# Kernel optimization log

Hardware: AMD Instinct MI355X
Metric: run time of the kernel (lower is better)

Reference implementation:

```python
import jax, jax.numpy as jnp
import numpy as np

EMB = 384
RANK = 8


def feature2token(f):
    # [B,C,H,W] -> [B,HW,C]
    B, C, H, W = f.shape
    return f.reshape(B, C, H * W).transpose(0, 2, 1)


def token2feature(t, H, W):
    # [B,N,C] -> [B,C,H,W]
    B, N, C = t.shape
    return t.transpose(0, 2, 1).reshape(B, C, H, W)


def linear(t, w, b):
    # torch Linear: y = t @ w.T + b ; w: [out,in]
    return jnp.einsum('bnc,oc->bno', t, w) + b


def hard_mask(y_soft, k):
    # straight-through one-hot mask of the top-k entries of y_soft, per row
    B, N = y_soft.shape
    idx = jax.lax.top_k(y_soft, k)[1]                      # [B,k]
    y_hard = jnp.zeros_like(y_soft).at[jnp.arange(B)[:, None], idx].set(1.0)
    return y_hard - jax.lax.stop_gradient(y_soft) + y_soft


def gumbel_masks(scores, k):
    # scores: [B,N] raw logits; module applies log_softmax then softmax
    y_soft = jax.nn.softmax(jax.nn.log_softmax(scores, axis=-1), axis=-1)
    token_mask = hard_mask(y_soft, k)        # top-k
    rej_mask = hard_mask(-y_soft, k) + 2.0 * jax.lax.stop_gradient(y_soft) - 2.0 * y_soft
    # note: rej uses topk of (-y_soft) for indices but straight-through around +y_soft,
    # so compute it directly for clarity:
    B, N = y_soft.shape
    idx_bot = jax.lax.top_k(-y_soft, k)[1]
    y_hard_bot = jnp.zeros_like(y_soft).at[jnp.arange(B)[:, None], idx_bot].set(1.0)
    rej_mask = y_hard_bot - jax.lax.stop_gradient(y_soft) + y_soft
    return token_mask, rej_mask


def setup_inputs() -> dict:
    key = jax.random.key(0)
    ks = jax.random.split(key, 20)
    B, C, H, W = 32, EMB, 32, 32
    s_emb = 1.0 / np.sqrt(EMB)
    s_2r = 1.0 / np.sqrt(2 * RANK)
    s_r = 1.0 / np.sqrt(RANK)
    inp = {
        'x': jax.random.normal(ks[0], (B, 2 * C, H, W), jnp.float32),
        'gx_w': jax.random.uniform(ks[1], (1, EMB), jnp.float32, -s_emb, s_emb),
        'gx_b': jax.random.uniform(ks[2], (1,), jnp.float32, -s_emb, s_emb),
        'gm_w': jax.random.uniform(ks[3], (1, EMB), jnp.float32, -s_emb, s_emb),
        'gm_b': jax.random.uniform(ks[4], (1,), jnp.float32, -s_emb, s_emb),
        'px_w': jax.random.uniform(ks[5], (RANK, EMB), jnp.float32, -s_emb, s_emb),
        'px_b': jax.random.uniform(ks[6], (RANK,), jnp.float32, -s_emb, s_emb),
        'pm_w': jax.random.uniform(ks[7], (RANK, EMB), jnp.float32, -s_emb, s_emb),
        'pm_b': jax.random.uniform(ks[8], (RANK,), jnp.float32, -s_emb, s_emb),
        'prx_w': jax.random.uniform(ks[9], (RANK, EMB), jnp.float32, -s_emb, s_emb),
        'prx_b': jax.random.uniform(ks[10], (RANK,), jnp.float32, -s_emb, s_emb),
        'prm_w': jax.random.uniform(ks[11], (RANK, EMB), jnp.float32, -s_emb, s_emb),
        'prm_b': jax.random.uniform(ks[12], (RANK,), jnp.float32, -s_emb, s_emb),
        'pfx_w': jax.random.uniform(ks[13], (RANK, 2 * RANK), jnp.float32, -s_2r, s_2r),
        'pfx_b': jax.random.uniform(ks[14], (RANK,), jnp.float32, -s_2r, s_2r),
        'pfm_w': jax.random.uniform(ks[15], (RANK, 2 * RANK), jnp.float32, -s_2r, s_2r),
        'pfm_b': jax.random.uniform(ks[16], (RANK,), jnp.float32, -s_2r, s_2r),
        'pb_w': jax.random.uniform(ks[17], (EMB, RANK), jnp.float32, -s_r, s_r),
        'pb_b': jax.random.uniform(ks[18], (EMB,), jnp.float32, -s_r, s_r),
    }
    return inp


def reference(x, gx_w, gx_b, gm_w, gm_b, px_w, px_b, pm_w, pm_b,
              prx_w, prx_b, prm_w, prm_b, pfx_w, pfx_b, pfm_w, pfm_b,
              pb_w, pb_b):
    xh, modh = jnp.split(x, 2, axis=1)           # each [B,C,H,W]
    H, W = xh.shape[2], xh.shape[3]
    xt = feature2token(xh)                        # [B,N,C]
    mt = feature2token(modh)
    B, N, _ = xt.shape
    k = N // 4

    # x-branch
    scores_x = linear(xt, gx_w, gx_b).reshape(B, N)
    tm_x, rm_x = gumbel_masks(scores_x, k)
    tm_x, rm_x = tm_x[..., None], rm_x[..., None]             # [B,N,1] broadcast over emb
    low_x = linear(xt * tm_x + mt * rm_x, px_w, px_b)
    low_res_x = linear((xt + mt) * (1.0 - rm_x - tm_x), prx_w, prx_b)
    fuse_x = linear(jnp.concatenate([low_x, low_res_x], axis=2), pfx_w, pfx_b)

    # mod-branch
    scores_m = linear(mt, gm_w, gm_b).reshape(B, N)
    tm_m, rm_m = gumbel_masks(scores_m, k)
    tm_m, rm_m = tm_m[..., None], rm_m[..., None]
    low_m = linear(mt * tm_m + xt * rm_m, pm_w, pm_b)
    low_res_m = linear((xt + mt) * (1.0 - rm_m - tm_m), prm_w, prm_b)
    fuse_m = linear(jnp.concatenate([low_m, low_res_m], axis=2), pfm_w, pfm_b)

    fuse = linear(fuse_x + fuse_m, pb_w, pb_b)   # [B,N,EMB]
    return token2feature(fuse, H, W)
```

## Files before the change

### kernel.cpp

```cpp
#include <hip/hip_runtime.h>

#define NTOK 1024
#define KSEL 256


template <int CS>
__global__ __launch_bounds__(128) void k1_proj(
    const float* __restrict__ x,
    const float* __restrict__ gx_w, const float* __restrict__ gm_w,
    const float* __restrict__ px_w, const float* __restrict__ pm_w,
    const float* __restrict__ prx_w, const float* __restrict__ prm_w,
    float* __restrict__ Pp)
{
  constexpr int NS = 384 / CS;
  constexpr int SB = (NS == 1) ? 0 : 2;
  constexpr int NCB = CS / 16;
  int blk = blockIdx.x;
  int part = blk & 1;
  int ntile = (blk >> 1) & 7;
  int s = (blk >> 4) & (NS - 1);
  int b = blk >> (4 + SB);
  int n = ntile * 128 + threadIdx.x;
  const float* gw = part ? gm_w : gx_w;
  int cw0 = s * CS;

  float acc[33];
  #pragma unroll
  for (int j = 0; j < 33; ++j) acc[j] = 0.f;

  const float* xp = x + ((size_t)b * 768 + part * 384 + cw0) * NTOK + n;

  float cur[16], nxt[16];
  #pragma unroll
  for (int i = 0; i < 16; ++i) cur[i] = xp[(size_t)i * NTOK];

  #pragma unroll
  for (int cb = 0; cb < NCB; ++cb) {
    #pragma unroll
    for (int i = 0; i < 16; ++i)
      nxt[i] = (cb + 1 < NCB) ? xp[(size_t)((cb + 1) * 16 + i) * NTOK] : 0.f;
    #pragma unroll
    for (int i = 0; i < 16; ++i) {
      int cw = cw0 + cb * 16 + i;
      float v = cur[i];
      acc[0] = fmaf(gw[cw], v, acc[0]);
      #pragma unroll
      for (int r = 0; r < 8; ++r) {
        acc[1 + r]  = fmaf(px_w[r * 384 + cw],  v, acc[1 + r]);
        acc[9 + r]  = fmaf(pm_w[r * 384 + cw],  v, acc[9 + r]);
        acc[17 + r] = fmaf(prx_w[r * 384 + cw], v, acc[17 + r]);
        acc[25 + r] = fmaf(prm_w[r * 384 + cw], v, acc[25 + r]);
      }
    }
    #pragma unroll
    for (int i = 0; i < 16; ++i) cur[i] = nxt[i];
  }
  float* op = Pp + ((((size_t)s * 32 + b) * 2 + part) * 33) * NTOK + n;
  #pragma unroll
  for (int j = 0; j < 33; ++j) op[(size_t)j * NTOK] = acc[j];
}

__global__ __launch_bounds__(64) void k2_masks(
    const float* __restrict__ Ppart, float* __restrict__ masks, int nsplit)
{
  int b = blockIdx.x >> 1;
  int branch = blockIdx.x & 1;
  int lane = threadIdx.x;
  unsigned long long lmask = (1ull << lane) - 1ull;

  float v[16];
  #pragma unroll
  for (int i = 0; i < 16; ++i) v[i] = 0.f;
  for (int s = 0; s < nsplit; ++s) {
    const float* sp = Ppart + (((size_t)s * 32 + b) * 2 + branch) * 33 * NTOK;
    #pragma unroll
    for (int i = 0; i < 16; ++i) v[i] += sp[i * 64 + lane];
  }
  unsigned key[16];
  #pragma unroll
  for (int i = 0; i < 16; ++i) {
    float f = v[i] + 0.0f;
    unsigned bits = __float_as_uint(f);
    key[i] = (bits & 0x80000000u) ? ~bits : (bits | 0x80000000u);
  }

  for (int which = 0; which < 2; ++which) {
    unsigned prefix = 0u;
    for (int bit = 31; bit >= 0; --bit) {
      unsigned cand = prefix | (1u << bit);
      int cnt = 0;
      #pragma unroll
      for (int i = 0; i < 16; ++i) {
        unsigned kk = which ? ~key[i] : key[i];
        cnt += __popcll(__ballot(kk >= cand));
      }
      if (cnt >= KSEL) prefix = cand;
    }
    int cgt = 0;
    #pragma unroll
    for (int i = 0; i < 16; ++i) {
      unsigned kk = which ? ~key[i] : key[i];
      cgt += __popcll(__ballot(kk > prefix));
    }
    int quota = KSEL - cgt;
    float* mp = masks + ((size_t)b * 4 + branch * 2 + which) * NTOK;
    int run = 0;
    #pragma unroll
    for (int i = 0; i < 16; ++i) {
      unsigned kk = which ? ~key[i] : key[i];
      bool eq = (kk == prefix);
      unsigned long long bal = __ballot(eq);
      int rank = run + __popcll(bal & lmask);
      bool sel = (kk > prefix) || (eq && rank < quota);
      mp[i * 64 + lane] = sel ? 1.0f : 0.0f;
      run += __popcll(bal);
    }
  }
}

template <int NS>
__global__ __launch_bounds__(1024) void k3a(
    const float* __restrict__ Ppart, const float* __restrict__ masks,
    const float* __restrict__ px_b, const float* __restrict__ pm_b,
    const float* __restrict__ prx_b, const float* __restrict__ prm_b,
    float* __restrict__ LOWS)
{
  int r = blockIdx.x & 7;
  int b = blockIdx.x >> 3;
  int n = threadIdx.x;

  float ax = 0.f, am = 0.f, bmv = 0.f, bxv = 0.f, cx = 0.f, cm = 0.f;
  #pragma unroll
  for (int s = 0; s < NS; ++s) {
    const float* P0 = Ppart + (((size_t)s * 32 + b) * 2 + 0) * 33 * NTOK + n;
    const float* P1 = Ppart + (((size_t)s * 32 + b) * 2 + 1) * 33 * NTOK + n;
    ax  += P0[(size_t)(1 + r) * NTOK];
    am  += P1[(size_t)(1 + r) * NTOK];
    bmv += P0[(size_t)(9 + r) * NTOK];
    bxv += P1[(size_t)(9 + r) * NTOK];
    cx  += P0[(size_t)(17 + r) * NTOK] + P1[(size_t)(17 + r) * NTOK];
    cm  += P0[(size_t)(25 + r) * NTOK] + P1[(size_t)(25 + r) * NTOK];
  }
  const float* mk = masks + (size_t)b * 4 * NTOK + n;
  float tmx = mk[0 * NTOK], rmx = mk[1 * NTOK];
  float tmm = mk[2 * NTOK], rmm = mk[3 * NTOK];
  float wx = 1.0f - tmx - rmx;
  float wm = 1.0f - tmm - rmm;

  float lowx = fmaf(tmx, ax, fmaf(rmx, am, px_b[r]));
  float lrx  = fmaf(wx, cx, prx_b[r]);
  float lowm = fmaf(tmm, bxv, fmaf(rmm, bmv, pm_b[r]));
  float lrm  = fmaf(wm, cm, prm_b[r]);

  float* L = LOWS + ((size_t)b * 32 + r) * NTOK + n;
  L[0 * 8 * NTOK] = lowx;
  L[1 * 8 * NTOK] = lrx;
  L[2 * 8 * NTOK] = lowm;
  L[3 * 8 * NTOK] = lrm;
}

__global__ __launch_bounds__(1024) void k3b(
    const float* __restrict__ LOWS,
    const float* __restrict__ pfx_w, const float* __restrict__ pfx_b,
    const float* __restrict__ pfm_w, const float* __restrict__ pfm_b,
    float* __restrict__ G)
{
  int b = blockIdx.x;
  int n = threadIdx.x;
  const float* L = LOWS + (size_t)b * 32 * NTOK + n;
  float lowx[8], lrx[8], lowm[8], lrm[8];
  #pragma unroll
  for (int r = 0; r < 8; ++r) {
    lowx[r] = L[(size_t)(0 * 8 + r) * NTOK];
    lrx[r]  = L[(size_t)(1 * 8 + r) * NTOK];
    lowm[r] = L[(size_t)(2 * 8 + r) * NTOK];
    lrm[r]  = L[(size_t)(3 * 8 + r) * NTOK];
  }
  float g[8];
  #pragma unroll
  for (int r = 0; r < 8; ++r) {
    float acc = pfx_b[r] + pfm_b[r];
    #pragma unroll
    for (int s2 = 0; s2 < 8; ++s2) {
      acc = fmaf(pfx_w[r * 16 + s2],     lowx[s2], acc);
      acc = fmaf(pfx_w[r * 16 + 8 + s2], lrx[s2],  acc);
      acc = fmaf(pfm_w[r * 16 + s2],     lowm[s2], acc);
      acc = fmaf(pfm_w[r * 16 + 8 + s2], lrm[s2],  acc);
    }
    g[r] = acc;
  }
  float4* Gp = reinterpret_cast<float4*>(G + ((size_t)b * NTOK + n) * 8);
  Gp[0] = make_float4(g[0], g[1], g[2], g[3]);
  Gp[1] = make_float4(g[4], g[5], g[6], g[7]);
}

__global__ __launch_bounds__(64) void k4_out(
    const float* __restrict__ G, const float* __restrict__ pb_w,
    const float* __restrict__ pb_b, float* __restrict__ out)
{
  int blk = blockIdx.x;
  int ttile = blk & 3;
  int cpart = (blk >> 2) & 3;
  int b = blk >> 4;
  int n0 = ttile * 256 + threadIdx.x * 4;

  const float4* Gp = reinterpret_cast<const float4*>(G + ((size_t)b * NTOK + n0) * 8);
  float4 ga0 = Gp[0], ga1 = Gp[1];
  float4 gb0 = Gp[2], gb1 = Gp[3];
  float4 gc0 = Gp[4], gc1 = Gp[5];
  float4 gd0 = Gp[6], gd1 = Gp[7];

  float* op = out + ((size_t)b * 384 + (size_t)cpart * 96) * NTOK + n0;
  const float* wp = pb_w + (size_t)cpart * 96 * 8;
  const float* bp = pb_b + (size_t)cpart * 96;
  #pragma unroll 4
  for (int c = 0; c < 96; ++c) {
    const float* w = wp + c * 8;
    float w0 = w[0], w1 = w[1], w2 = w[2], w3 = w[3];
    float w4 = w[4], w5 = w[5], w6 = w[6], w7 = w[7];
    float bb = bp[c];
    float4 o;
    o.x = bb; o.y = bb; o.z = bb; o.w = bb;
    o.x = fmaf(w0, ga0.x, o.x); o.x = fmaf(w1, ga0.y, o.x);
    o.x = fmaf(w2, ga0.z, o.x); o.x = fmaf(w3, ga0.w, o.x);
    o.x = fmaf(w4, ga1.x, o.x); o.x = fmaf(w5, ga1.y, o.x);
    o.x = fmaf(w6, ga1.z, o.x); o.x = fmaf(w7, ga1.w, o.x);
    o.y = fmaf(w0, gb0.x, o.y); o.y = fmaf(w1, gb0.y, o.y);
    o.y = fmaf(w2, gb0.z, o.y); o.y = fmaf(w3, gb0.w, o.y);
    o.y = fmaf(w4, gb1.x, o.y); o.y = fmaf(w5, gb1.y, o.y);
    o.y = fmaf(w6, gb1.z, o.y); o.y = fmaf(w7, gb1.w, o.y);
    o.z = fmaf(w0, gc0.x, o.z); o.z = fmaf(w1, gc0.y, o.z);
    o.z = fmaf(w2, gc0.z, o.z); o.z = fmaf(w3, gc0.w, o.z);
    o.z = fmaf(w4, gc1.x, o.z); o.z = fmaf(w5, gc1.y, o.z);
    o.z = fmaf(w6, gc1.z, o.z); o.z = fmaf(w7, gc1.w, o.z);
    o.w = fmaf(w0, gd0.x, o.w); o.w = fmaf(w1, gd0.y, o.w);
    o.w = fmaf(w2, gd0.z, o.w); o.w = fmaf(w3, gd0.w, o.w);
    o.w = fmaf(w4, gd1.x, o.w); o.w = fmaf(w5, gd1.y, o.w);
    o.w = fmaf(w6, gd1.z, o.w); o.w = fmaf(w7, gd1.w, o.w);
    *reinterpret_cast<float4*>(op + (size_t)c * NTOK) = o;
  }
}

extern "C" void kernel_launch(void* const* d_in, const int* in_sizes, int n_in,
                              void* d_out, int out_size, void* d_ws, size_t ws_size,
                              hipStream_t stream) {
  const float* x     = (const float*)d_in[0];
  const float* gx_w  = (const float*)d_in[1];
  const float* gm_w  = (const float*)d_in[3];
  const float* px_w  = (const float*)d_in[5];
  const float* px_b  = (const float*)d_in[6];
  const float* pm_w  = (const float*)d_in[7];
  const float* pm_b  = (const float*)d_in[8];
  const float* prx_w = (const float*)d_in[9];
  const float* prx_b = (const float*)d_in[10];
  const float* prm_w = (const float*)d_in[11];
  const float* prm_b = (const float*)d_in[12];
  const float* pfx_w = (const float*)d_in[13];
  const float* pfx_b = (const float*)d_in[14];
  const float* pfm_w = (const float*)d_in[15];
  const float* pfm_b = (const float*)d_in[16];
  const float* pb_w  = (const float*)d_in[17];
  const float* pb_b  = (const float*)d_in[18];
  float* out = (float*)d_out;

  const size_t P1_F   = 32ull * 2 * 33 * NTOK;
  const size_t MASK_F = 32ull * 4 * NTOK;
  const size_t G_F    = 32ull * NTOK * 8;
  const size_t LOWS_F = 32ull * 32 * NTOK;
  const size_t need4  = (4 * P1_F + MASK_F + G_F + LOWS_F) * 4;

  float* ws = (float*)d_ws;
  if (ws_size >= need4) {
    float* Ppart = ws;
    float* masks = ws + 4 * P1_F;
    float* G     = masks + MASK_F;
    float* LOWS  = G + G_F;
    k1_proj<96><<<2048, 128, 0, stream>>>(x, gx_w, gm_w, px_w, pm_w, prx_w, prm_w, Ppart);
    k2_masks<<<64, 64, 0, stream>>>(Ppart, masks, 4);
    k3a<4><<<256, 1024, 0, stream>>>(Ppart, masks, px_b, pm_b, prx_b, prm_b, LOWS);
    k3b<<<32, 1024, 0, stream>>>(LOWS, pfx_w, pfx_b, pfm_w, pfm_b, G);
    k4_out<<<512, 64, 0, stream>>>(G, pb_w, pb_b, out);
  } else {
    float* Ppart = ws;
    float* masks = ws + P1_F;
    float* G     = masks + MASK_F;
    float* LOWS  = G + G_F;
    k1_proj<384><<<512, 128, 0, stream>>>(x, gx_w, gm_w, px_w, pm_w, prx_w, prm_w, Ppart);
    k2_masks<<<64, 64, 0, stream>>>(Ppart, masks, 1);
    k3a<1><<<256, 1024, 0, stream>>>(Ppart, masks, px_b, pm_b, prx_b, prm_b, LOWS);
    k3b<<<32, 1024, 0, stream>>>(LOWS, pfx_w, pfx_b, pfm_w, pfm_b, G);
    k4_out<<<512, 64, 0, stream>>>(G, pb_w, pb_b, out);
  }
}
```

Baseline: 300.2 us.

## Stage projection weights in LDS, split channels 8-way, fuse k3b into output kernel

The first projection kernel now stages its 33xCS weight slice in shared memory and reads it as float4, replacing scalar global weight loads, and adds an 8-way channel split when the workspace allows it. k3a moves to 256-thread blocks over token tiles. k3b and k4_out are merged into one kernel that computes the 8-wide fused vector per token and writes the 384 output channels directly, removing the G buffer round trip. The cost is more partial-sum traffic and reduction work from the 8-way split, and redundant recomputation of g across the four channel-part blocks.

```diff
diff --git a/kernel.cpp b/kernel.cpp
--- a/kernel.cpp
+++ b/kernel.cpp
@@ -4,7 +4,7 @@
 #define KSEL 256
 
 
-template <int CS>
+template <int NS>
 __global__ __launch_bounds__(128) void k1_proj(
     const float* __restrict__ x,
     const float* __restrict__ gx_w, const float* __restrict__ gm_w,
@@ -12,9 +12,10 @@
     const float* __restrict__ prx_w, const float* __restrict__ prm_w,
     float* __restrict__ Pp)
 {
-  constexpr int NS = 384 / CS;
-  constexpr int SB = (NS == 1) ? 0 : 2;
-  constexpr int NCB = CS / 16;
+  constexpr int CS = 384 / NS;
+  constexpr int SB = (NS == 8) ? 3 : (NS == 4) ? 2 : 0;
+  __shared__ float wlds[33 * CS];
+
   int blk = blockIdx.x;
   int part = blk & 1;
   int ntile = (blk >> 1) & 7;
@@ -24,36 +25,38 @@
   const float* gw = part ? gm_w : gx_w;
   int cw0 = s * CS;
 
+  for (int idx = threadIdx.x; idx < 33 * CS; idx += 128) {
+    int j = idx / CS;
+    int c = idx - j * CS;
+    const float* src;
+    if (j == 0)       src = gw + cw0;
+    else if (j < 9)   src = px_w  + (j - 1)  * 384 + cw0;
+    else if (j < 17)  src = pm_w  + (j - 9)  * 384 + cw0;
+    else if (j < 25)  src = prx_w + (j - 17) * 384 + cw0;
+    else              src = prm_w + (j - 25) * 384 + cw0;
+    wlds[idx] = src[c];
+  }
+  __syncthreads();
+
   float acc[33];
   #pragma unroll
   for (int j = 0; j < 33; ++j) acc[j] = 0.f;
 
   const float* xp = x + ((size_t)b * 768 + part * 384 + cw0) * NTOK + n;
-
-  float cur[16], nxt[16];
-  #pragma unroll
-  for (int i = 0; i < 16; ++i) cur[i] = xp[(size_t)i * NTOK];
-
-  #pragma unroll
-  for (int cb = 0; cb < NCB; ++cb) {
-    #pragma unroll
-    for (int i = 0; i < 16; ++i)
-      nxt[i] = (cb + 1 < NCB) ? xp[(size_t)((cb + 1) * 16 + i) * NTOK] : 0.f;
-    #pragma unroll
-    for (int i = 0; i < 16; ++i) {
-      int cw = cw0 + cb * 16 + i;
-      float v = cur[i];
-      acc[0] = fmaf(gw[cw], v, acc[0]);
-      #pragma unroll
-      for (int r = 0; r < 8; ++r) {
-        acc[1 + r]  = fmaf(px_w[r * 384 + cw],  v, acc[1 + r]);
-        acc[9 + r]  = fmaf(pm_w[r * 384 + cw],  v, acc[9 + r]);
-        acc[17 + r] = fmaf(prx_w[r * 384 + cw], v, acc[17 + r]);
-        acc[25 + r] = fmaf(prm_w[r * 384 + cw], v, acc[25 + r]);
-      }
-    }
-    #pragma unroll
-    for (int i = 0; i < 16; ++i) cur[i] = nxt[i];
+  #pragma unroll 2
+  for (int c4 = 0; c4 < CS / 4; ++c4) {
+    float v0 = xp[(size_t)(c4 * 4 + 0) * NTOK];
+    float v1 = xp[(size_t)(c4 * 4 + 1) * NTOK];
+    float v2 = xp[(size_t)(c4 * 4 + 2) * NTOK];
+    float v3 = xp[(size_t)(c4 * 4 + 3) * NTOK];
+    #pragma unroll
+    for (int j = 0; j < 33; ++j) {
+      float4 w = *reinterpret_cast<const float4*>(&wlds[j * CS + c4 * 4]);
+      acc[j] = fmaf(w.x, v0, acc[j]);
+      acc[j] = fmaf(w.y, v1, acc[j]);
+      acc[j] = fmaf(w.z, v2, acc[j]);
+      acc[j] = fmaf(w.w, v3, acc[j]);
+    }
   }
   float* op = Pp + ((((size_t)s * 32 + b) * 2 + part) * 33) * NTOK + n;
   #pragma unroll
@@ -119,15 +122,16 @@
 }
 
 template <int NS>
-__global__ __launch_bounds__(1024) void k3a(
+__global__ __launch_bounds__(256) void k3a(
     const float* __restrict__ Ppart, const float* __restrict__ masks,
     const float* __restrict__ px_b, const float* __restrict__ pm_b,
     const float* __restrict__ prx_b, const float* __restrict__ prm_b,
     float* __restrict__ LOWS)
 {
-  int r = blockIdx.x & 7;
-  int b = blockIdx.x >> 3;
-  int n = threadIdx.x;
+  int ttile = blockIdx.x & 3;
+  int r = (blockIdx.x >> 2) & 7;
+  int b = blockIdx.x >> 5;
+  int n = ttile * 256 + threadIdx.x;
 
   float ax = 0.f, am = 0.f, bmv = 0.f, bxv = 0.f, cx = 0.f, cm = 0.f;
   #pragma unroll
@@ -159,85 +163,59 @@
   L[3 * 8 * NTOK] = lrm;
 }
 
-__global__ __launch_bounds__(1024) void k3b(
+__global__ __launch_bounds__(64) void k4f(
     const float* __restrict__ LOWS,
     const float* __restrict__ pfx_w, const float* __restrict__ pfx_b,
     const float* __restrict__ pfm_w, const float* __restrict__ pfm_b,
-    float* __restrict__ G)
-{
-  int b = blockIdx.x;
-  int n = threadIdx.x;
-  const float* L = LOWS + (size_t)b * 32 * NTOK + n;
-  float lowx[8], lrx[8], lowm[8], lrm[8];
-  #pragma unroll
-  for (int r = 0; r < 8; ++r) {
-    lowx[r] = L[(size_t)(0 * 8 + r) * NTOK];
-    lrx[r]  = L[(size_t)(1 * 8 + r) * NTOK];
-    lowm[r] = L[(size_t)(2 * 8 + r) * NTOK];
-    lrm[r]  = L[(size_t)(3 * 8 + r) * NTOK];
-  }
-  float g[8];
-  #pragma unroll
-  for (int r = 0; r < 8; ++r) {
-    float acc = pfx_b[r] + pfm_b[r];
-    #pragma unroll
-    for (int s2 = 0; s2 < 8; ++s2) {
-      acc = fmaf(pfx_w[r * 16 + s2],     lowx[s2], acc);
-      acc = fmaf(pfx_w[r * 16 + 8 + s2], lrx[s2],  acc);
-      acc = fmaf(pfm_w[r * 16 + s2],     lowm[s2], acc);
-      acc = fmaf(pfm_w[r * 16 + 8 + s2], lrm[s2],  acc);
-    }
-    g[r] = acc;
-  }
-  float4* Gp = reinterpret_cast<float4*>(G + ((size_t)b * NTOK + n) * 8);
-  Gp[0] = make_float4(g[0], g[1], g[2], g[3]);
-  Gp[1] = make_float4(g[4], g[5], g[6], g[7]);
-}
-
-__global__ __launch_bounds__(64) void k4_out(
-    const float* __restrict__ G, const float* __restrict__ pb_w,
-    const float* __restrict__ pb_b, float* __restrict__ out)
+    const float* __restrict__ pb_w, const float* __restrict__ pb_b,
+    float* __restrict__ out)
 {
   int blk = blockIdx.x;
   int ttile = blk & 3;
   int cpart = (blk >> 2) & 3;
   int b = blk >> 4;
-  int n0 = ttile * 256 + threadIdx.x * 4;
-
-  const float4* Gp = reinterpret_cast<const float4*>(G + ((size_t)b * NTOK + n0) * 8);
-  float4 ga0 = Gp[0], ga1 = Gp[1];
-  float4 gb0 = Gp[2], gb1 = Gp[3];
-  float4 gc0 = Gp[4], gc1 = Gp[5];
-  float4 gd0 = Gp[6], gd1 = Gp[7];
-
-  float* op = out + ((size_t)b * 384 + (size_t)cpart * 96) * NTOK + n0;
+  int lane = threadIdx.x;
+
   const float* wp = pb_w + (size_t)cpart * 96 * 8;
   const float* bp = pb_b + (size_t)cpart * 96;
-  #pragma unroll 4
-  for (int c = 0; c < 96; ++c) {
-    const float* w = wp + c * 8;
-    float w0 = w[0], w1 = w[1], w2 = w[2], w3 = w[3];
-    float w4 = w[4], w5 = w[5], w6 = w[6], w7 = w[7];
-    float bb = bp[c];
-    float4 o;
-    o.x = bb; o.y = bb; o.z = bb; o.w = bb;
-    o.x = fmaf(w0, ga0.x, o.x); o.x = fmaf(w1, ga0.y, o.x);
-    o.x = fmaf(w2, ga0.z, o.x); o.x = fmaf(w3, ga0.w, o.x);
-    o.x = fmaf(w4, ga1.x, o.x); o.x = fmaf(w5, ga1.y, o.x);
-    o.x = fmaf(w6, ga1.z, o.x); o.x = fmaf(w7, ga1.w, o.x);
-    o.y = fmaf(w0, gb0.x, o.y); o.y = fmaf(w1, gb0.y, o.y);
-    o.y = fmaf(w2, gb0.z, o.y); o.y = fmaf(w3, gb0.w, o.y);
-    o.y = fmaf(w4, gb1.x, o.y); o.y = fmaf(w5, gb1.y, o.y);
-    o.y = fmaf(w6, gb1.z, o.y); o.y = fmaf(w7, gb1.w, o.y);
-    o.z = fmaf(w0, gc0.x, o.z); o.z = fmaf(w1, gc0.y, o.z);
-    o.z = fmaf(w2, gc0.z, o.z); o.z = fmaf(w3, gc0.w, o.z);
-    o.z = fmaf(w4, gc1.x, o.z); o.z = fmaf(w5, gc1.y, o.z);
-    o.z = fmaf(w6, gc1.z, o.z); o.z = fmaf(w7, gc1.w, o.z);
-    o.w = fmaf(w0, gd0.x, o.w); o.w = fmaf(w1, gd0.y, o.w);
-    o.w = fmaf(w2, gd0.z, o.w); o.w = fmaf(w3, gd0.w, o.w);
-    o.w = fmaf(w4, gd1.x, o.w); o.w = fmaf(w5, gd1.y, o.w);
-    o.w = fmaf(w6, gd1.z, o.w); o.w = fmaf(w7, gd1.w, o.w);
-    *reinterpret_cast<float4*>(op + (size_t)c * NTOK) = o;
+
+  #pragma unroll
+  for (int t = 0; t < 4; ++t) {
+    int n = ttile * 256 + t * 64 + lane;
+    const float* L = LOWS + (size_t)b * 32 * NTOK + n;
+    float lows[32];
+    #pragma unroll
+    for (int i = 0; i < 32; ++i) lows[i] = L[(size_t)i * NTOK];
+
+    float g[8];
+    #pragma unroll
+    for (int r = 0; r < 8; ++r) {
+      float acc = pfx_b[r] + pfm_b[r];
+      #pragma unroll
+      for (int s2 = 0; s2 < 8; ++s2) {
+        acc = fmaf(pfx_w[r * 16 + s2],     lows[s2],      acc);
+        acc = fmaf(pfx_w[r * 16 + 8 + s2], lows[8 + s2],  acc);
+        acc = fmaf(pfm_w[r * 16 + s2],     lows[16 + s2], acc);
+        acc = fmaf(pfm_w[r * 16 + 8 + s2], lows[24 + s2], acc);
+      }
+      g[r] = acc;
+    }
+
+    float* op = out + ((size_t)b * 384 + (size_t)cpart * 96) * NTOK + n;
+    #pragma unroll 4
+    for (int c = 0; c < 96; ++c) {
+      const float* w = wp + c * 8;
+      float acc = bp[c];
+      acc = fmaf(w[0], g[0], acc);
+      acc = fmaf(w[1], g[1], acc);
+      acc = fmaf(w[2], g[2], acc);
+      acc = fmaf(w[3], g[3], acc);
+      acc = fmaf(w[4], g[4], acc);
+      acc = fmaf(w[5], g[5], acc);
+      acc = fmaf(w[6], g[6], acc);
+      acc = fmaf(w[7], g[7], acc);
+      op[(size_t)c * NTOK] = acc;
+    }
   }
 }
 
@@ -265,30 +243,34 @@
 
   const size_t P1_F   = 32ull * 2 * 33 * NTOK;
   const size_t MASK_F = 32ull * 4 * NTOK;
-  const size_t G_F    = 32ull * NTOK * 8;
   const size_t LOWS_F = 32ull * 32 * NTOK;
-  const size_t need4  = (4 * P1_F + MASK_F + G_F + LOWS_F) * 4;
+  const size_t need8  = (8 * P1_F + MASK_F + LOWS_F) * 4;
+  const size_t need4  = (4 * P1_F + MASK_F + LOWS_F) * 4;
 
   float* ws = (float*)d_ws;
-  if (ws_size >= need4) {
+  if (ws_size >= need8) {
+    float* Ppart = ws;
+    float* masks = ws + 8 * P1_F;
+    float* LOWS  = masks + MASK_F;
+    k1_proj<8><<<4096, 128, 0, stream>>>(x, gx_w, gm_w, px_w, pm_w, prx_w, prm_w, Ppart);
+    k2_masks<<<64, 64, 0, stream>>>(Ppart, masks, 8);
+    k3a<8><<<1024, 256, 0, stream>>>(Ppart, masks, px_b, pm_b, prx_b, prm_b, LOWS);
+    k4f<<<512, 64, 0, stream>>>(LOWS, pfx_w, pfx_b, pfm_w, pfm_b, pb_w, pb_b, out);
+  } else if (ws_size >= need4) {
     float* Ppart = ws;
     float* masks = ws + 4 * P1_F;
-    float* G     = masks + MASK_F;
-    float* LOWS  = G + G_F;
-    k1_proj<96><<<2048, 128, 0, stream>>>(x, gx_w, gm_w, px_w, pm_w, prx_w, prm_w, Ppart);
+    float* LOWS  = masks + MASK_F;
+    k1_proj<4><<<2048, 128, 0, stream>>>(x, gx_w, gm_w, px_w, pm_w, prx_w, prm_w, Ppart);
     k2_masks<<<64, 64, 0, stream>>>(Ppart, masks, 4);
-    k3a<4><<<256, 1024, 0, stream>>>(Ppart, masks, px_b, pm_b, prx_b, prm_b, LOWS);
-    k3b<<<32, 1024, 0, stream>>>(LOWS, pfx_w, pfx_b, pfm_w, pfm_b, G);
-    k4_out<<<512, 64, 0, stream>>>(G, pb_w, pb_b, out);
+    k3a<4><<<1024, 256, 0, stream>>>(Ppart, masks, px_b, pm_b, prx_b, prm_b, LOWS);
+    k4f<<<512, 64, 0, stream>>>(LOWS, pfx_w, pfx_b, pfm_w, pfm_b, pb_w, pb_b, out);
   } else {
     float* Ppart = ws;
     float* masks = ws + P1_F;
-    float* G     = masks + MASK_F;
-    float* LOWS  = G + G_F;
-    k1_proj<384><<<512, 128, 0, stream>>>(x, gx_w, gm_w, px_w, pm_w, prx_w, prm_w, Ppart);
+    float* LOWS  = masks + MASK_F;
+    k1_proj<1><<<512, 128, 0, stream>>>(x, gx_w, gm_w, px_w, pm_w, prx_w, prm_w, Ppart);
     k2_masks<<<64, 64, 0, stream>>>(Ppart, masks, 1);
-    k3a<1><<<256, 1024, 0, stream>>>(Ppart, masks, px_b, pm_b, prx_b, prm_b, LOWS);
-    k3b<<<32, 1024, 0, stream>>>(LOWS, pfx_w, pfx_b, pfm_w, pfm_b, G);
-    k4_out<<<512, 64, 0, stream>>>(G, pb_w, pb_b, out);
-  }
-}
+    k3a<1><<<1024, 256, 0, stream>>>(Ppart, masks, px_b, pm_b, prx_b, prm_b, LOWS);
+    k4f<<<512, 64, 0, stream>>>(LOWS, pfx_w, pfx_b, pfm_w, pfm_b, pb_w, pb_b, out);
+  }
+}
```

After: 280.2 us. 6.7% less time.
